# Optimization experiments

Hardware: AMD Instinct MI355X
Metric: run time of the kernel (lower is better)

The kernel has to match this reference:

```python
import jax, jax.numpy as jnp
import numpy as np

B, T, C = 4, 2048, 1024
H = 16
D = C // H  # head_dim = 64

def setup_inputs() -> dict:
    key = jax.random.key(0)
    k1, k2, k3 = jax.random.split(key, 3)
    s = 1.0 / np.sqrt(C)
    x = jax.random.normal(k1, (B, T, C), dtype=jnp.float32)
    w_qkv = jax.random.normal(k2, (C, 3 * C), dtype=jnp.float32) * s
    w_proj = jax.random.normal(k3, (C, C), dtype=jnp.float32) * s
    b_proj = jnp.zeros((C,), dtype=jnp.float32)
    return {"x": x, "w_qkv": w_qkv, "w_proj": w_proj, "b_proj": b_proj}

def reference(x, w_qkv, w_proj, b_proj):
    Bc, Tc, Cc = x.shape
    scale = 1.0 / np.sqrt(D)
    qkv = x @ w_qkv                       # [B,T,3C]
    q, k, v = jnp.split(qkv, 3, axis=-1)  # each [B,T,C]
    def heads(t):
        return t.reshape(Bc, Tc, H, D).transpose(0, 2, 1, 3)  # [B,H,T,D]
    q, k, v = heads(q), heads(k), heads(v)
    attn = jnp.einsum('bhqd,bhkd->bhqk', q, k) * scale        # [B,H,T,T]
    causal = jnp.tril(jnp.ones((Tc, Tc), dtype=bool))
    attn = jnp.where(causal, attn, -jnp.inf)
    attn = jax.nn.softmax(attn, axis=-1)
    out = jnp.einsum('bhqk,bhkd->bhqd', attn, v)              # [B,H,T,D]
    out = out.transpose(0, 2, 1, 3).reshape(Bc, Tc, Cc)
    return out @ w_proj + b_proj
```

## Files before the change

### kernel.cpp

```cpp
#include <hip/hip_runtime.h>

typedef unsigned short u16;
typedef unsigned int u32;
typedef __attribute__((ext_vector_type(8))) __bf16 bf16x8;
typedef __attribute__((ext_vector_type(4))) float f32x4;
typedef __attribute__((ext_vector_type(16))) float f32x16;
typedef __attribute__((ext_vector_type(8))) unsigned short ushort8;
typedef __attribute__((ext_vector_type(4))) unsigned short ushort4v;
typedef __attribute__((ext_vector_type(4))) unsigned int u32x4;
typedef __attribute__((ext_vector_type(4))) float float4v;

#define B_ 4
#define T_ 2048
#define C_ 1024
#define H_ 16
#define D_ 64
#define M_ (B_ * T_)

union ABUn { ushort8 u; bf16x8 b; };

__device__ __forceinline__ u16 f2bf(float f) {
  u32 u = __builtin_bit_cast(u32, f);
  u32 r = u + 0x7fffu + ((u >> 16) & 1u);
  return (u16)(r >> 16);
}

__device__ __forceinline__ float fexp2(float x) {
  float r; asm("v_exp_f32 %0, %1" : "=v"(r) : "v"(x)); return r;
}

__device__ __forceinline__ u32 pkbf(float lo, float hi_) {
  u32 r; asm("v_cvt_pk_bf16_f32 %0, %1, %2" : "=v"(r) : "v"(lo), "v"(hi_)); return r;
}

__device__ __forceinline__ void gl16(const u16* g, u16* l) {
  __builtin_amdgcn_global_load_lds((const __attribute__((address_space(1))) void*)g,
                                   (__attribute__((address_space(3))) void*)l, 16, 0, 0);
}

__global__ void cast_kernel(const float* __restrict__ in, u16* __restrict__ out, int n4) {
  int i = blockIdx.x * blockDim.x + threadIdx.x;
  if (i >= n4) return;
  float4v v = ((const float4v*)in)[i];
  ushort4v o;
  o[0] = f2bf(v[0]); o[1] = f2bf(v[1]); o[2] = f2bf(v[2]); o[3] = f2bf(v[3]);
  ((ushort4v*)out)[i] = o;
}

__global__ void transpose_cast_kernel(const float* __restrict__ src, u16* __restrict__ dst,
                                      int Kd, int Nd) {
  __shared__ float tile[32][33];
  int n0 = blockIdx.x * 32, k0 = blockIdx.y * 32;
  int tx = threadIdx.x, ty = threadIdx.y;
#pragma unroll
  for (int i = 0; i < 32; i += 8)
    tile[ty + i][tx] = src[(k0 + ty + i) * Nd + n0 + tx];
  __syncthreads();
#pragma unroll
  for (int i = 0; i < 32; i += 8)
    dst[(n0 + ty + i) * Kd + k0 + tx] = f2bf(tile[tx][ty + i]);
}

template <int EPI>
__global__ __launch_bounds__(256, 2) void gemm_bt(
    const u16* __restrict__ A, const u16* __restrict__ Bt,
    u16* __restrict__ Qb, u16* __restrict__ Kb, u16* __restrict__ Vb,
    float* __restrict__ Out, const float* __restrict__ bias) {
  __shared__ u16 As[128 * 64];
  __shared__ u16 Bs[128 * 64];
  const int tid = threadIdx.x;
  const int lane = tid & 63, wave = tid >> 6;
  const int wm = wave >> 1, wn = wave & 1;
  const int lg = lane >> 4, lr = lane & 15;
  const int m0 = blockIdx.y * 128, n0 = blockIdx.x * 128;

  f32x4 acc[4][4];
  const f32x4 zero = {0.0f, 0.0f, 0.0f, 0.0f};
#pragma unroll
  for (int mi = 0; mi < 4; ++mi)
#pragma unroll
    for (int ni = 0; ni < 4; ++ni) acc[mi][ni] = zero;

  const u16* Abase = A + m0 * 1024;
  const u16* Bbase = Bt + n0 * 1024;
  int aoff[4];
#pragma unroll
  for (int j = 0; j < 4; ++j) {
    int s = wave * 256 + j * 64 + lane;
    int row = s >> 3, sp = s & 7;
    aoff[j] = row * 1024 + (sp ^ (row & 7)) * 8;
  }
  char* AsB = (char*)As;
  char* BsB = (char*)Bs;

  for (int k0 = 0; k0 < 1024; k0 += 64) {
#pragma unroll
    for (int j = 0; j < 4; ++j) {
      u16* ldst_a = &As[(wave * 256 + j * 64) * 8];
      u16* ldst_b = &Bs[(wave * 256 + j * 64) * 8];
      gl16(Abase + aoff[j] + k0, ldst_a);
      gl16(Bbase + aoff[j] + k0, ldst_b);
    }
    __syncthreads();
#pragma unroll
    for (int kk = 0; kk < 2; ++kk) {
      bf16x8 am[4], bn[4];
#pragma unroll
      for (int mi = 0; mi < 4; ++mi) {
        int row = wm * 64 + mi * 16 + lr;
        ABUn u;
        u.u = *(const ushort8*)(AsB + ((u32)(row * 128 + ((kk * 64 + lg * 16) ^ ((row & 7) << 4)))));
        am[mi] = u.b;
      }
#pragma unroll
      for (int ni = 0; ni < 4; ++ni) {
        int row = wn * 64 + ni * 16 + lr;
        ABUn u;
        u.u = *(const ushort8*)(BsB + ((u32)(row * 128 + ((kk * 64 + lg * 16) ^ ((row & 7) << 4)))));
        bn[ni] = u.b;
      }
#pragma unroll
      for (int mi = 0; mi < 4; ++mi)
#pragma unroll
        for (int ni = 0; ni < 4; ++ni)
          acc[mi][ni] = __builtin_amdgcn_mfma_f32_16x16x32_bf16(am[mi], bn[ni], acc[mi][ni], 0, 0, 0);
    }
    __syncthreads();
  }

#pragma unroll
  for (int mi = 0; mi < 4; ++mi)
#pragma unroll
    for (int ni = 0; ni < 4; ++ni) {
      int m = m0 + wm * 64 + mi * 16 + lg * 4;
      int n = n0 + wn * 64 + ni * 16 + lr;
      if (EPI == 0) {
        int part = n >> 10, c = n & 1023;
        int h = c >> 6, d = c & 63;
        int b = m >> 11, t = m & 2047;
        if (part == 2) {
          ushort4v pv;
#pragma unroll
          for (int r = 0; r < 4; ++r) pv[r] = f2bf(acc[mi][ni][r]);
          *(ushort4v*)&Vb[((b * H_ + h) * D_ + d) * T_ + t] = pv;
        } else {
#pragma unroll
          for (int r = 0; r < 4; ++r) {
            float v = acc[mi][ni][r];
            if (part == 0)
              Qb[((b * H_ + h) * T_ + t + r) * D_ + d] = f2bf(v * 0.18033688f);
            else
              Kb[((b * H_ + h) * T_ + t + r) * D_ + d] = f2bf(v);
          }
        }
      } else {
#pragma unroll
        for (int r = 0; r < 4; ++r)
          Out[(m + r) * 1024 + n] = acc[mi][ni][r] + bias[n];
      }
    }
}

__global__ __launch_bounds__(256, 4) void attn_kernel(
    const u16* __restrict__ Qb, const u16* __restrict__ Kb,
    const u16* __restrict__ Vt, u16* __restrict__ Ob) {
  __shared__ u16 smem[4][4096];
  const int bh = blockIdx.y;
  const int q0 = (15 - (int)blockIdx.x) * 128;
  const int tid = threadIdx.x;
  const int lane = tid & 63, wave = tid >> 6;
  const int hi = lane >> 5, ln = lane & 31;
  const int qw0 = q0 + wave * 32;
  const int hh = bh & (H_ - 1), bb = bh >> 4;

  const u16* Qh = Qb + bh * (T_ * D_);
  const u16* Kh = Kb + bh * (T_ * D_);
  const u16* Vh = Vt + bh * (T_ * D_);

  bf16x8 qf[4];
  {
    const u16* qr = Qh + (qw0 + ln) * 64 + hi * 8;
#pragma unroll
    for (int ks = 0; ks < 4; ++ks)
      qf[ks] = __builtin_bit_cast(bf16x8, *(const ushort8*)(qr + ks * 16));
  }

  f32x16 o[2];
#pragma unroll
  for (int dt = 0; dt < 2; ++dt)
#pragma unroll
    for (int i = 0; i < 16; ++i) o[dt][i] = 0.0f;
  float m = -1e30f, l = 0.0f;

  const int nchunk = q0 / 64 + 2;
  const int slot0 = wave * 128;

#pragma unroll
  for (int j = 0; j < 2; ++j) {
    int slot = slot0 + j * 64 + lane;
    int r = slot >> 3, sp = slot & 7;
    int sl = sp ^ (r & 7);
    gl16(Kh + r * 64 + sl * 8, &smem[0][(slot0 + j * 64) * 8]);
    gl16(Vh + r * 2048 + sl * 8, &smem[2][(slot0 + j * 64) * 8]);
  }
  __syncthreads();

  for (int ch = 0; ch < nchunk; ++ch) {
    const int kv0 = ch * 64;
    const int cur = ch & 1;
    if (ch + 1 < nchunk) {
      const int kn = kv0 + 64;
#pragma unroll
      for (int j = 0; j < 2; ++j) {
        int slot = slot0 + j * 64 + lane;
        int r = slot >> 3, sp = slot & 7;
        int sl = sp ^ (r & 7);
        gl16(Kh + (kn + r) * 64 + sl * 8, &smem[cur ^ 1][(slot0 + j * 64) * 8]);
        gl16(Vh + r * 2048 + kn + sl * 8, &smem[2 + (cur ^ 1)][(slot0 + j * 64) * 8]);
      }
    }
    if (kv0 <= qw0 + 31) {
      const char* Kc = (const char*)smem[cur];
      const char* Vc = (const char*)smem[2 + cur];
      f32x16 s0, s1;
#pragma unroll
      for (int i = 0; i < 16; ++i) { s0[i] = 0.0f; s1[i] = 0.0f; }
      __builtin_amdgcn_s_setprio(1);
#pragma unroll
      for (int ks = 0; ks < 4; ++ks) {
        int r0 = ln, r1 = 32 + ln;
        bf16x8 kf0 = __builtin_bit_cast(bf16x8,
            *(const ushort8*)(Kc + r0 * 128 + (u32)((ks * 32 + hi * 16) ^ ((r0 & 7) << 4))));
        bf16x8 kf1 = __builtin_bit_cast(bf16x8,
            *(const ushort8*)(Kc + r1 * 128 + (u32)((ks * 32 + hi * 16) ^ ((r1 & 7) << 4))));
        s0 = __builtin_amdgcn_mfma_f32_32x32x16_bf16(kf0, qf[ks], s0, 0, 0, 0);
        s1 = __builtin_amdgcn_mfma_f32_32x32x16_bf16(kf1, qf[ks], s1, 0, 0, 0);
      }
      __builtin_amdgcn_s_setprio(0);

      const int qg = qw0 + ln;
      if ((kv0 + 63) > qw0) {
#pragma unroll
        for (int r = 0; r < 16; ++r) {
          int R = (r & 3) + 8 * (r >> 2) + 4 * hi;
          s0[r] = (kv0 + R > qg) ? -1e30f : s0[r];
          s1[r] = (kv0 + 32 + R > qg) ? -1e30f : s1[r];
        }
      }
      float mx[8];
#pragma unroll
      for (int i = 0; i < 8; ++i)
        mx[i] = fmaxf(fmaxf(s0[i], s0[i + 8]), fmaxf(s1[i], s1[i + 8]));
#pragma unroll
      for (int i = 0; i < 4; ++i) mx[i] = fmaxf(mx[i], mx[i + 4]);
      float cm = fmaxf(fmaxf(mx[0], mx[1]), fmaxf(mx[2], mx[3]));
      cm = fmaxf(cm, __shfl_xor(cm, 32));
      float mn = fmaxf(m, cm);
      float fsc = fexp2(m - mn);
      m = mn;
#pragma unroll
      for (int r = 0; r < 16; ++r) {
        s0[r] = fexp2(s0[r] - mn);
        s1[r] = fexp2(s1[r] - mn);
      }
      float sm[8];
#pragma unroll
      for (int i = 0; i < 8; ++i) sm[i] = (s0[i] + s0[i + 8]) + (s1[i] + s1[i + 8]);
#pragma unroll
      for (int i = 0; i < 4; ++i) sm[i] += sm[i + 4];
      float ssum = (sm[0] + sm[1]) + (sm[2] + sm[3]);
      ssum += __shfl_xor(ssum, 32);
      l = l * fsc + ssum;
#pragma unroll
      for (int dt = 0; dt < 2; ++dt)
#pragma unroll
        for (int i = 0; i < 16; ++i) o[dt][i] *= fsc;

      bf16x8 pb[4];
#pragma unroll
      for (int sub = 0; sub < 2; ++sub) {
        u32 a0, a1, a2, a3, a4, a5, a6, a7;
        if (sub == 0) {
          a0 = pkbf(s0[0], s0[1]);  a1 = pkbf(s0[2], s0[3]);
          a2 = pkbf(s0[4], s0[5]);  a3 = pkbf(s0[6], s0[7]);
          a4 = pkbf(s0[8], s0[9]);  a5 = pkbf(s0[10], s0[11]);
          a6 = pkbf(s0[12], s0[13]); a7 = pkbf(s0[14], s0[15]);
        } else {
          a0 = pkbf(s1[0], s1[1]);  a1 = pkbf(s1[2], s1[3]);
          a2 = pkbf(s1[4], s1[5]);  a3 = pkbf(s1[6], s1[7]);
          a4 = pkbf(s1[8], s1[9]);  a5 = pkbf(s1[10], s1[11]);
          a6 = pkbf(s1[12], s1[13]); a7 = pkbf(s1[14], s1[15]);
        }
        u32 x0 = __shfl_xor(hi ? a0 : a2, 32);
        u32 x1 = __shfl_xor(hi ? a1 : a3, 32);
        u32 x2 = __shfl_xor(hi ? a4 : a6, 32);
        u32 x3 = __shfl_xor(hi ? a5 : a7, 32);
        u32x4 w0, w1;
        w0[0] = hi ? x0 : a0; w0[1] = hi ? x1 : a1;
        w0[2] = hi ? a2 : x0; w0[3] = hi ? a3 : x1;
        w1[0] = hi ? x2 : a4; w1[1] = hi ? x3 : a5;
        w1[2] = hi ? a6 : x2; w1[3] = hi ? a7 : x3;
        pb[sub * 2 + 0] = __builtin_bit_cast(bf16x8, w0);
        pb[sub * 2 + 1] = __builtin_bit_cast(bf16x8, w1);
      }
      __builtin_amdgcn_s_setprio(1);
#pragma unroll
      for (int dt = 0; dt < 2; ++dt) {
        int r = dt * 32 + ln;
        u32 rs = (u32)((r & 7) << 4);
#pragma unroll
        for (int ks = 0; ks < 4; ++ks) {
          bf16x8 vfk = __builtin_bit_cast(bf16x8,
              *(const ushort8*)(Vc + r * 128 + (u32)((ks * 32 + hi * 16) ^ rs)));
          o[dt] = __builtin_amdgcn_mfma_f32_32x32x16_bf16(vfk, pb[ks], o[dt], 0, 0, 0);
        }
      }
      __builtin_amdgcn_s_setprio(0);
    }
    __syncthreads();
  }

  __syncthreads();
  char* Wb = (char*)smem[wave];
  {
    float inv = 1.0f / l;
    int q = ln;
    u32 rs = (u32)((q & 7) << 4);
#pragma unroll
    for (int dt = 0; dt < 2; ++dt)
#pragma unroll
      for (int p = 0; p < 8; ++p) {
        u32 w = pkbf(o[dt][2 * p] * inv, o[dt][2 * p + 1] * inv);
        int d = dt * 32 + ((2 * p) & 3) + 8 * (p >> 1) + 4 * hi;
        *(u32*)(Wb + ((u32)(q * 128 + d * 2) ^ rs)) = w;
      }
  }
#pragma unroll
  for (int j = 0; j < 4; ++j) {
    int idx = j * 64 + lane;
    int row = idx >> 3, sp = idx & 7;
    ushort8 v = *(const ushort8*)(Wb + row * 128 + (u32)((sp * 16) ^ ((row & 7) << 4)));
    *(ushort8*)(Ob + (bb * T_ + qw0 + row) * C_ + hh * 64 + sp * 8) = v;
  }
}

extern "C" void kernel_launch(void* const* d_in, const int* in_sizes, int n_in,
                              void* d_out, int out_size, void* d_ws, size_t ws_size,
                              hipStream_t stream) {
  const float* x = (const float*)d_in[0];
  const float* w_qkv = (const float*)d_in[1];
  const float* w_proj = (const float*)d_in[2];
  const float* b_proj = (const float*)d_in[3];
  float* out = (float*)d_out;

  char* ws = (char*)d_ws;
  u16* xb = (u16*)(ws);
  u16* wqT = (u16*)(ws + 16777216);
  u16* wpT = (u16*)(ws + 16777216 + 6291456);
  u16* Qb = (u16*)(ws + 25165824);
  u16* Kb = (u16*)(ws + 25165824 + 16777216);
  u16* Vt = (u16*)(ws + 25165824 + 2 * 16777216);
  u16* Ob = xb;

  cast_kernel<<<(M_ * C_ / 4 + 255) / 256, 256, 0, stream>>>(x, xb, M_ * C_ / 4);
  dim3 tb(32, 8);
  transpose_cast_kernel<<<dim3(3 * C_ / 32, C_ / 32), tb, 0, stream>>>(w_qkv, wqT, C_, 3 * C_);
  transpose_cast_kernel<<<dim3(C_ / 32, C_ / 32), tb, 0, stream>>>(w_proj, wpT, C_, C_);

  gemm_bt<0><<<dim3(3 * C_ / 128, M_ / 128), 256, 0, stream>>>(
      xb, wqT, Qb, Kb, Vt, nullptr, nullptr);

  attn_kernel<<<dim3(T_ / 128, B_ * H_), 256, 0, stream>>>(Qb, Kb, Vt, Ob);

  gemm_bt<1><<<dim3(C_ / 128, M_ / 128), 256, 0, stream>>>(
      Ob, wpT, nullptr, nullptr, nullptr, out, b_proj);
}
```

Measured before the change: 280.6 us.

## Pair causal query tiles per block for load balance; use permlane32 swap

```diff
diff --git a/kernel.cpp b/kernel.cpp
--- a/kernel.cpp
+++ b/kernel.cpp
@@ -166,181 +166,187 @@
     const u16* __restrict__ Vt, u16* __restrict__ Ob) {
   __shared__ u16 smem[4][4096];
   const int bh = blockIdx.y;
-  const int q0 = (15 - (int)blockIdx.x) * 128;
   const int tid = threadIdx.x;
   const int lane = tid & 63, wave = tid >> 6;
   const int hi = lane >> 5, ln = lane & 31;
-  const int qw0 = q0 + wave * 32;
   const int hh = bh & (H_ - 1), bb = bh >> 4;
 
   const u16* Qh = Qb + bh * (T_ * D_);
   const u16* Kh = Kb + bh * (T_ * D_);
   const u16* Vh = Vt + bh * (T_ * D_);
-
-  bf16x8 qf[4];
-  {
-    const u16* qr = Qh + (qw0 + ln) * 64 + hi * 8;
-#pragma unroll
-    for (int ks = 0; ks < 4; ++ks)
-      qf[ks] = __builtin_bit_cast(bf16x8, *(const ushort8*)(qr + ks * 16));
-  }
-
-  f32x16 o[2];
-#pragma unroll
-  for (int dt = 0; dt < 2; ++dt)
-#pragma unroll
-    for (int i = 0; i < 16; ++i) o[dt][i] = 0.0f;
-  float m = -1e30f, l = 0.0f;
-
-  const int nchunk = q0 / 64 + 2;
   const int slot0 = wave * 128;
 
+  int srow[2], scol[2];
 #pragma unroll
   for (int j = 0; j < 2; ++j) {
     int slot = slot0 + j * 64 + lane;
-    int r = slot >> 3, sp = slot & 7;
-    int sl = sp ^ (r & 7);
-    gl16(Kh + r * 64 + sl * 8, &smem[0][(slot0 + j * 64) * 8]);
-    gl16(Vh + r * 2048 + sl * 8, &smem[2][(slot0 + j * 64) * 8]);
+    srow[j] = slot >> 3;
+    scol[j] = (slot & 7) ^ (srow[j] & 7);
   }
-  __syncthreads();
-
-  for (int ch = 0; ch < nchunk; ++ch) {
-    const int kv0 = ch * 64;
-    const int cur = ch & 1;
-    if (ch + 1 < nchunk) {
-      const int kn = kv0 + 64;
-#pragma unroll
-      for (int j = 0; j < 2; ++j) {
-        int slot = slot0 + j * 64 + lane;
-        int r = slot >> 3, sp = slot & 7;
-        int sl = sp ^ (r & 7);
-        gl16(Kh + (kn + r) * 64 + sl * 8, &smem[cur ^ 1][(slot0 + j * 64) * 8]);
-        gl16(Vh + r * 2048 + kn + sl * 8, &smem[2 + (cur ^ 1)][(slot0 + j * 64) * 8]);
-      }
-    }
-    if (kv0 <= qw0 + 31) {
-      const char* Kc = (const char*)smem[cur];
-      const char* Vc = (const char*)smem[2 + cur];
-      f32x16 s0, s1;
-#pragma unroll
-      for (int i = 0; i < 16; ++i) { s0[i] = 0.0f; s1[i] = 0.0f; }
-      __builtin_amdgcn_s_setprio(1);
-#pragma unroll
-      for (int ks = 0; ks < 4; ++ks) {
-        int r0 = ln, r1 = 32 + ln;
-        bf16x8 kf0 = __builtin_bit_cast(bf16x8,
-            *(const ushort8*)(Kc + r0 * 128 + (u32)((ks * 32 + hi * 16) ^ ((r0 & 7) << 4))));
-        bf16x8 kf1 = __builtin_bit_cast(bf16x8,
-            *(const ushort8*)(Kc + r1 * 128 + (u32)((ks * 32 + hi * 16) ^ ((r1 & 7) << 4))));
-        s0 = __builtin_amdgcn_mfma_f32_32x32x16_bf16(kf0, qf[ks], s0, 0, 0, 0);
-        s1 = __builtin_amdgcn_mfma_f32_32x32x16_bf16(kf1, qf[ks], s1, 0, 0, 0);
-      }
-      __builtin_amdgcn_s_setprio(0);
-
-      const int qg = qw0 + ln;
-      if ((kv0 + 63) > qw0) {
+
+#pragma unroll
+  for (int pass = 0; pass < 2; ++pass) {
+    const int q0 = pass ? (1920 - (int)blockIdx.x * 128) : ((int)blockIdx.x * 128);
+    const int qw0 = q0 + wave * 32;
+
+    bf16x8 qf[4];
+    {
+      const u16* qr = Qh + (qw0 + ln) * 64 + hi * 8;
+#pragma unroll
+      for (int ks = 0; ks < 4; ++ks)
+        qf[ks] = __builtin_bit_cast(bf16x8, *(const ushort8*)(qr + ks * 16));
+    }
+
+    f32x16 o[2];
+#pragma unroll
+    for (int dt = 0; dt < 2; ++dt)
+#pragma unroll
+      for (int i = 0; i < 16; ++i) o[dt][i] = 0.0f;
+    float m = -1e30f, l = 0.0f;
+
+    const int nchunk = q0 / 64 + 2;
+
+    __syncthreads();
+#pragma unroll
+    for (int j = 0; j < 2; ++j) {
+      gl16(Kh + srow[j] * 64 + scol[j] * 8, &smem[0][(slot0 + j * 64) * 8]);
+      gl16(Vh + srow[j] * 2048 + scol[j] * 8, &smem[2][(slot0 + j * 64) * 8]);
+    }
+    __syncthreads();
+
+    for (int ch = 0; ch < nchunk; ++ch) {
+      const int kv0 = ch * 64;
+      const int cur = ch & 1;
+      if (ch + 1 < nchunk) {
+        const int kn = kv0 + 64;
+#pragma unroll
+        for (int j = 0; j < 2; ++j) {
+          gl16(Kh + (kn + srow[j]) * 64 + scol[j] * 8, &smem[cur ^ 1][(slot0 + j * 64) * 8]);
+          gl16(Vh + srow[j] * 2048 + kn + scol[j] * 8, &smem[2 + (cur ^ 1)][(slot0 + j * 64) * 8]);
+        }
+      }
+      if (kv0 <= qw0 + 31) {
+        const char* Kc = (const char*)smem[cur];
+        const char* Vc = (const char*)smem[2 + cur];
+        f32x16 s0, s1;
+#pragma unroll
+        for (int i = 0; i < 16; ++i) { s0[i] = 0.0f; s1[i] = 0.0f; }
+        __builtin_amdgcn_s_setprio(1);
+#pragma unroll
+        for (int ks = 0; ks < 4; ++ks) {
+          int r0 = ln, r1 = 32 + ln;
+          bf16x8 kf0 = __builtin_bit_cast(bf16x8,
+              *(const ushort8*)(Kc + r0 * 128 + (u32)((ks * 32 + hi * 16) ^ ((r0 & 7) << 4))));
+          bf16x8 kf1 = __builtin_bit_cast(bf16x8,
+              *(const ushort8*)(Kc + r1 * 128 + (u32)((ks * 32 + hi * 16) ^ ((r1 & 7) << 4))));
+          s0 = __builtin_amdgcn_mfma_f32_32x32x16_bf16(kf0, qf[ks], s0, 0, 0, 0);
+          s1 = __builtin_amdgcn_mfma_f32_32x32x16_bf16(kf1, qf[ks], s1, 0, 0, 0);
+        }
+        __builtin_amdgcn_s_setprio(0);
+
+        const int qg = qw0 + ln;
+        if ((kv0 + 63) > qw0) {
+#pragma unroll
+          for (int r = 0; r < 16; ++r) {
+            int R = (r & 3) + 8 * (r >> 2) + 4 * hi;
+            s0[r] = (kv0 + R > qg) ? -1e30f : s0[r];
+            s1[r] = (kv0 + 32 + R > qg) ? -1e30f : s1[r];
+          }
+        }
+        float mx[8];
+#pragma unroll
+        for (int i = 0; i < 8; ++i)
+          mx[i] = fmaxf(fmaxf(s0[i], s0[i + 8]), fmaxf(s1[i], s1[i + 8]));
+#pragma unroll
+        for (int i = 0; i < 4; ++i) mx[i] = fmaxf(mx[i], mx[i + 4]);
+        float cm = fmaxf(fmaxf(mx[0], mx[1]), fmaxf(mx[2], mx[3]));
+        cm = fmaxf(cm, __shfl_xor(cm, 32));
+        float mn = fmaxf(m, cm);
+        float fsc = fexp2(m - mn);
+        m = mn;
 #pragma unroll
         for (int r = 0; r < 16; ++r) {
-          int R = (r & 3) + 8 * (r >> 2) + 4 * hi;
-          s0[r] = (kv0 + R > qg) ? -1e30f : s0[r];
-          s1[r] = (kv0 + 32 + R > qg) ? -1e30f : s1[r];
-        }
-      }
-      float mx[8];
-#pragma unroll
-      for (int i = 0; i < 8; ++i)
-        mx[i] = fmaxf(fmaxf(s0[i], s0[i + 8]), fmaxf(s1[i], s1[i + 8]));
-#pragma unroll
-      for (int i = 0; i < 4; ++i) mx[i] = fmaxf(mx[i], mx[i + 4]);
-      float cm = fmaxf(fmaxf(mx[0], mx[1]), fmaxf(mx[2], mx[3]));
-      cm = fmaxf(cm, __shfl_xor(cm, 32));
-      float mn = fmaxf(m, cm);
-      float fsc = fexp2(m - mn);
-      m = mn;
-#pragma unroll
-      for (int r = 0; r < 16; ++r) {
-        s0[r] = fexp2(s0[r] - mn);
-        s1[r] = fexp2(s1[r] - mn);
-      }
-      float sm[8];
-#pragma unroll
-      for (int i = 0; i < 8; ++i) sm[i] = (s0[i] + s0[i + 8]) + (s1[i] + s1[i + 8]);
-#pragma unroll
-      for (int i = 0; i < 4; ++i) sm[i] += sm[i + 4];
-      float ssum = (sm[0] + sm[1]) + (sm[2] + sm[3]);
-      ssum += __shfl_xor(ssum, 32);
-      l = l * fsc + ssum;
+          s0[r] = fexp2(s0[r] - mn);
+          s1[r] = fexp2(s1[r] - mn);
+        }
+        float sm[8];
+#pragma unroll
+        for (int i = 0; i < 8; ++i) sm[i] = (s0[i] + s0[i + 8]) + (s1[i] + s1[i + 8]);
+#pragma unroll
+        for (int i = 0; i < 4; ++i) sm[i] += sm[i + 4];
+        float ssum = (sm[0] + sm[1]) + (sm[2] + sm[3]);
+        ssum += __shfl_xor(ssum, 32);
+        l = l * fsc + ssum;
+#pragma unroll
+        for (int dt = 0; dt < 2; ++dt)
+#pragma unroll
+          for (int i = 0; i < 16; ++i) o[dt][i] *= fsc;
+
+        bf16x8 pb[4];
+#pragma unroll
+        for (int sub = 0; sub < 2; ++sub) {
+          u32 a0, a1, a2, a3, a4, a5, a6, a7;
+          if (sub == 0) {
+            a0 = pkbf(s0[0], s0[1]);  a1 = pkbf(s0[2], s0[3]);
+            a2 = pkbf(s0[4], s0[5]);  a3 = pkbf(s0[6], s0[7]);
+            a4 = pkbf(s0[8], s0[9]);  a5 = pkbf(s0[10], s0[11]);
+            a6 = pkbf(s0[12], s0[13]); a7 = pkbf(s0[14], s0[15]);
+          } else {
+            a0 = pkbf(s1[0], s1[1]);  a1 = pkbf(s1[2], s1[3]);
+            a2 = pkbf(s1[4], s1[5]);  a3 = pkbf(s1[6], s1[7]);
+            a4 = pkbf(s1[8], s1[9]);  a5 = pkbf(s1[10], s1[11]);
+            a6 = pkbf(s1[12], s1[13]); a7 = pkbf(s1[14], s1[15]);
+          }
+          asm volatile("v_permlane32_swap_b32 %0, %1" : "+v"(a0), "+v"(a2));
+          asm volatile("v_permlane32_swap_b32 %0, %1" : "+v"(a1), "+v"(a3));
+          asm volatile("v_permlane32_swap_b32 %0, %1" : "+v"(a4), "+v"(a6));
+          asm volatile("v_permlane32_swap_b32 %0, %1" : "+v"(a5), "+v"(a7));
+          u32x4 w0, w1;
+          w0[0] = a0; w0[1] = a1; w0[2] = a2; w0[3] = a3;
+          w1[0] = a4; w1[1] = a5; w1[2] = a6; w1[3] = a7;
+          pb[sub * 2 + 0] = __builtin_bit_cast(bf16x8, w0);
+          pb[sub * 2 + 1] = __builtin_bit_cast(bf16x8, w1);
+        }
+        __builtin_amdgcn_s_setprio(1);
+#pragma unroll
+        for (int dt = 0; dt < 2; ++dt) {
+          int r = dt * 32 + ln;
+          u32 rs = (u32)((r & 7) << 4);
+#pragma unroll
+          for (int ks = 0; ks < 4; ++ks) {
+            bf16x8 vfk = __builtin_bit_cast(bf16x8,
+                *(const ushort8*)(Vc + r * 128 + (u32)((ks * 32 + hi * 16) ^ rs)));
+            o[dt] = __builtin_amdgcn_mfma_f32_32x32x16_bf16(vfk, pb[ks], o[dt], 0, 0, 0);
+          }
+        }
+        __builtin_amdgcn_s_setprio(0);
+      }
+      __syncthreads();
+    }
+
+    __syncthreads();
+    char* Wb = (char*)smem[wave];
+    {
+      float inv = 1.0f / l;
+      int q = ln;
+      u32 rs = (u32)((q & 7) << 4);
 #pragma unroll
       for (int dt = 0; dt < 2; ++dt)
 #pragma unroll
-        for (int i = 0; i < 16; ++i) o[dt][i] *= fsc;
-
-      bf16x8 pb[4];
-#pragma unroll
-      for (int sub = 0; sub < 2; ++sub) {
-        u32 a0, a1, a2, a3, a4, a5, a6, a7;
-        if (sub == 0) {
-          a0 = pkbf(s0[0], s0[1]);  a1 = pkbf(s0[2], s0[3]);
-          a2 = pkbf(s0[4], s0[5]);  a3 = pkbf(s0[6], s0[7]);
-          a4 = pkbf(s0[8], s0[9]);  a5 = pkbf(s0[10], s0[11]);
-          a6 = pkbf(s0[12], s0[13]); a7 = pkbf(s0[14], s0[15]);
-        } else {
-          a0 = pkbf(s1[0], s1[1]);  a1 = pkbf(s1[2], s1[3]);
-          a2 = pkbf(s1[4], s1[5]);  a3 = pkbf(s1[6], s1[7]);
-          a4 = pkbf(s1[8], s1[9]);  a5 = pkbf(s1[10], s1[11]);
-          a6 = pkbf(s1[12], s1[13]); a7 = pkbf(s1[14], s1[15]);
-        }
-        u32 x0 = __shfl_xor(hi ? a0 : a2, 32);
-        u32 x1 = __shfl_xor(hi ? a1 : a3, 32);
-        u32 x2 = __shfl_xor(hi ? a4 : a6, 32);
-        u32 x3 = __shfl_xor(hi ? a5 : a7, 32);
-        u32x4 w0, w1;
-        w0[0] = hi ? x0 : a0; w0[1] = hi ? x1 : a1;
-        w0[2] = hi ? a2 : x0; w0[3] = hi ? a3 : x1;
-        w1[0] = hi ? x2 : a4; w1[1] = hi ? x3 : a5;
-        w1[2] = hi ? a6 : x2; w1[3] = hi ? a7 : x3;
-        pb[sub * 2 + 0] = __builtin_bit_cast(bf16x8, w0);
-        pb[sub * 2 + 1] = __builtin_bit_cast(bf16x8, w1);
-      }
-      __builtin_amdgcn_s_setprio(1);
-#pragma unroll
-      for (int dt = 0; dt < 2; ++dt) {
-        int r = dt * 32 + ln;
-        u32 rs = (u32)((r & 7) << 4);
-#pragma unroll
-        for (int ks = 0; ks < 4; ++ks) {
-          bf16x8 vfk = __builtin_bit_cast(bf16x8,
-              *(const ushort8*)(Vc + r * 128 + (u32)((ks * 32 + hi * 16) ^ rs)));
-          o[dt] = __builtin_amdgcn_mfma_f32_32x32x16_bf16(vfk, pb[ks], o[dt], 0, 0, 0);
-        }
-      }
-      __builtin_amdgcn_s_setprio(0);
-    }
-    __syncthreads();
-  }
-
-  __syncthreads();
-  char* Wb = (char*)smem[wave];
-  {
-    float inv = 1.0f / l;
-    int q = ln;
-    u32 rs = (u32)((q & 7) << 4);
-#pragma unroll
-    for (int dt = 0; dt < 2; ++dt)
-#pragma unroll
-      for (int p = 0; p < 8; ++p) {
-        u32 w = pkbf(o[dt][2 * p] * inv, o[dt][2 * p + 1] * inv);
-        int d = dt * 32 + ((2 * p) & 3) + 8 * (p >> 1) + 4 * hi;
-        *(u32*)(Wb + ((u32)(q * 128 + d * 2) ^ rs)) = w;
-      }
-  }
-#pragma unroll
-  for (int j = 0; j < 4; ++j) {
-    int idx = j * 64 + lane;
-    int row = idx >> 3, sp = idx & 7;
-    ushort8 v = *(const ushort8*)(Wb + row * 128 + (u32)((sp * 16) ^ ((row & 7) << 4)));
-    *(ushort8*)(Ob + (bb * T_ + qw0 + row) * C_ + hh * 64 + sp * 8) = v;
+        for (int p = 0; p < 8; ++p) {
+          u32 w = pkbf(o[dt][2 * p] * inv, o[dt][2 * p + 1] * inv);
+          int d = dt * 32 + ((2 * p) & 3) + 8 * (p >> 1) + 4 * hi;
+          *(u32*)(Wb + ((u32)(q * 128 + d * 2) ^ rs)) = w;
+        }
+    }
+    asm volatile("s_waitcnt lgkmcnt(0)" ::: "memory");
+#pragma unroll
+    for (int j = 0; j < 4; ++j) {
+      int idx = j * 64 + lane;
+      int row = idx >> 3, sp = idx & 7;
+      ushort8 v = *(const ushort8*)(Wb + row * 128 + (u32)((sp * 16) ^ ((row & 7) << 4)));
+      *(ushort8*)(Ob + (bb * T_ + qw0 + row) * C_ + hh * 64 + sp * 8) = v;
+    }
   }
 }
 
@@ -370,7 +376,7 @@
   gemm_bt<0><<<dim3(3 * C_ / 128, M_ / 128), 256, 0, stream>>>(
       xb, wqT, Qb, Kb, Vt, nullptr, nullptr);
 
-  attn_kernel<<<dim3(T_ / 128, B_ * H_), 256, 0, stream>>>(Qb, Kb, Vt, Ob);
+  attn_kernel<<<dim3(T_ / 256, B_ * H_), 256, 0, stream>>>(Qb, Kb, Vt, Ob);
 
   gemm_bt<1><<<dim3(C_ / 128, M_ / 128), 256, 0, stream>>>(
       Ob, wpT, nullptr, nullptr, nullptr, out, b_proj);
```

After: 250.0 us. 10.9% less time.
